# Kernel optimization log

Hardware: AMD Instinct MI355X
Metric: run time of the kernel (lower is better)

The kernel has to match this reference:

```python
import jax, jax.numpy as jnp
import numpy as np

N = 100000      # movie nodes
F_IN = 1024     # input feature dim
H, D = 8, 16    # heads, per-head dim (hidden = 128)
C = H * D       # hidden_channels = 128
E = 600000      # edges per metapath
P = 3           # number of metapath edge types
OUT = 3         # classes
NEG_SLOPE = 0.2


def setup_inputs() -> dict:
    key = jax.random.key(0)
    ks = jax.random.split(key, 10)
    return {
        "x_movie": jax.random.normal(ks[0], (N, F_IN), jnp.float32),
        "edge_index": jax.random.randint(ks[1], (P, 2, E), 0, N, jnp.int64),
        "W_proj": jax.random.normal(ks[2], (F_IN, C), jnp.float32) / np.sqrt(F_IN),
        "b_proj": jnp.zeros((C,), jnp.float32),
        "a_src": jax.random.normal(ks[3], (P, H, D), jnp.float32) / np.sqrt(D),
        "a_dst": jax.random.normal(ks[4], (P, H, D), jnp.float32) / np.sqrt(D),
        "k_W": jax.random.normal(ks[5], (C, C), jnp.float32) / np.sqrt(C),
        "k_b": jnp.zeros((C,), jnp.float32),
        "q": jax.random.normal(ks[6], (C,), jnp.float32) / np.sqrt(C),
        "lin_W": jax.random.normal(ks[7], (C, OUT), jnp.float32) / np.sqrt(C),
        "lin_b": jnp.zeros((OUT,), jnp.float32),
    }


def _metapath_attn(edge, asrc, adst, h):
    # edge: [2,E] int; asrc/adst: [H,D]; h: [N,H,D] projected node features
    n = h.shape[0]
    src, dst = edge[0], edge[1]
    al_s = (h * asrc).sum(-1)                 # [N,H]
    al_d = (h * adst).sum(-1)                 # [N,H]
    e = jax.nn.leaky_relu(al_s[src] + al_d[dst], NEG_SLOPE)  # [E,H]
    # per-destination softmax (numerically stable)
    m = jax.ops.segment_max(e, dst, num_segments=n)          # [N,H]
    p = jnp.exp(e - m[dst])
    denom = jax.ops.segment_sum(p, dst, num_segments=n)      # [N,H]
    alpha = p / (denom[dst] + 1e-16)                         # [E,H]
    msg = h[src] * alpha[..., None]                          # [E,H,D]
    out = jax.ops.segment_sum(msg, dst, num_segments=n)      # [N,H,D]
    return jax.nn.relu(out.reshape(n, H * D))                # [N,C]


def reference(x_movie, edge_index, W_proj, b_proj, a_src, a_dst, k_W, k_b, q, lin_W, lin_b):
    # shared node-type projection (dropout=0.6 omitted: eval mode)
    h = (x_movie @ W_proj + b_proj).reshape(N, H, D)         # [N,H,D]
    # per-metapath GAT attention, vmapped over the P metapath edge types
    outs = jax.vmap(_metapath_attn, in_axes=(0, 0, 0, None))(edge_index, a_src, a_dst, h)  # [P,N,C]
    # semantic attention fusion
    w = jnp.tanh(outs @ k_W + k_b).mean(axis=1)              # [P,C] mean over nodes
    score = (q * w).sum(-1)                                  # [P]
    beta = jax.nn.softmax(score)                             # [P]
    fused = (beta[:, None, None] * outs).sum(0)              # [N,C]
    return fused @ lin_W + lin_b                             # [N,OUT]
```

## Files before the change

### kernel.cpp

```cpp
#include <hip/hip_runtime.h>
#include <hip/hip_bf16.h>

#define NN 100000
#define FIN 1024
#define NH 8
#define ND 16
#define NC 128
#define NE 600000
#define NP 3
#define NOUT 3
#define NBLK 98

typedef __attribute__((ext_vector_type(8))) short bf16x8;
typedef __attribute__((ext_vector_type(4))) float f32x4;

__device__ __forceinline__ unsigned short f2bf(float f){
  union { __hip_bfloat16 b; unsigned short u; } cv;
  cv.b = __float2bfloat16(f);
  return cv.u;
}
__device__ __forceinline__ float bf2f(__hip_bfloat16 b){ return __bfloat162float(b); }
__device__ __forceinline__ float tanh_fast(float x){
  float e = __expf(2.0f*x);
  return 1.0f - 2.0f/(e + 1.0f);
}
__device__ __forceinline__ float lrelu(float x){ return x > 0.0f ? x : 0.2f*x; }

__global__ __launch_bounds__(256) void k_transpose_w(const float* __restrict__ W,
                                                     __hip_bfloat16* __restrict__ Wt){
  int t = blockIdx.x*256 + threadIdx.x;
  if (t >= FIN*NC) return;
  int k = t >> 7, c = t & 127;
  Wt[(size_t)c*FIN + k] = __float2bfloat16(W[t]);
}

__global__ __launch_bounds__(256) void k_proj(const float* __restrict__ x,
                                              const __hip_bfloat16* __restrict__ Wt,
                                              const float* __restrict__ bias,
                                              __hip_bfloat16* __restrict__ h){
  __shared__ __align__(16) __hip_bfloat16 As[64*40];
  __shared__ __align__(16) __hip_bfloat16 Bs[128*40];
  const int tid = threadIdx.x;
  const int wave = tid >> 6, lane = tid & 63;
  const int lr = lane & 15, lq = lane >> 4;
  const int m0 = blockIdx.x * 64;
  f32x4 acc[8] = {};
  for (int k0 = 0; k0 < FIN; k0 += 32){
#pragma unroll
    for (int i=0;i<2;i++){
      int idx = tid + 256*i;
      int row = idx >> 3, f4 = idx & 7;
      int gm = m0 + row; if (gm >= NN) gm = NN-1;
      const float4 v = *reinterpret_cast<const float4*>(x + (size_t)gm*FIN + k0 + f4*4);
      ushort4 pk; pk.x=f2bf(v.x); pk.y=f2bf(v.y); pk.z=f2bf(v.z); pk.w=f2bf(v.w);
      *reinterpret_cast<ushort4*>(&As[row*40 + f4*4]) = pk;
    }
#pragma unroll
    for (int i=0;i<2;i++){
      int idx = tid + 256*i;
      int c = idx >> 2, q = idx & 3;
      const uint4 v = *reinterpret_cast<const uint4*>(Wt + (size_t)c*FIN + k0 + q*8);
      *reinterpret_cast<uint4*>(&Bs[c*40 + q*8]) = v;
    }
    __syncthreads();
    bf16x8 afr = *reinterpret_cast<const bf16x8*>(&As[(wave*16 + lr)*40 + lq*8]);
#pragma unroll
    for (int t=0;t<8;t++){
      bf16x8 bfr = *reinterpret_cast<const bf16x8*>(&Bs[(t*16 + lr)*40 + lq*8]);
      acc[t] = __builtin_amdgcn_mfma_f32_16x16x32_bf16(afr, bfr, acc[t], 0, 0, 0);
    }
    __syncthreads();
  }
#pragma unroll
  for (int t=0;t<8;t++){
    int col = t*16 + lr;
    float bv = bias[col];
#pragma unroll
    for (int r=0;r<4;r++){
      int gm = m0 + wave*16 + lq*4 + r;
      if (gm < NN) h[(size_t)gm*NC + col] = __float2bfloat16(acc[t][r] + bv);
    }
  }
}

__global__ __launch_bounds__(256) void k_al(const __hip_bfloat16* __restrict__ h,
      const float* __restrict__ a_src, const float* __restrict__ a_dst,
      float* __restrict__ al_s, float* __restrict__ al_d){
  int t = blockIdx.x*256 + threadIdx.x;
  if (t >= NN*NH) return;
  int n = t >> 3, hh = t & 7;
  const __hip_bfloat16* hp = h + (size_t)n*NC + hh*ND;
  float hv[ND];
#pragma unroll
  for (int d=0; d<ND; d++) hv[d] = bf2f(hp[d]);
#pragma unroll
  for (int p=0;p<NP;p++){
    const float* as = a_src + (p*NH + hh)*ND;
    const float* ad = a_dst + (p*NH + hh)*ND;
    float ss=0.f, sd=0.f;
#pragma unroll
    for (int d=0;d<ND;d++){ ss += hv[d]*as[d]; sd += hv[d]*ad[d]; }
    al_s[((size_t)p*NN + n)*NH + hh] = ss;
    al_d[((size_t)p*NN + n)*NH + hh] = sd;
  }
}

__global__ __launch_bounds__(256) void k_deg(const int* __restrict__ edge,
                                             int* __restrict__ deg){
  int p = blockIdx.y;
  int e = blockIdx.x*256 + threadIdx.x;
  if (e >= NE) return;
  int dst = edge[(size_t)p*2*NE + NE + e];
  atomicAdd(&deg[p*NN + dst], 1);
}

__global__ __launch_bounds__(256) void k_scan_blk(const int* __restrict__ deg,
      int* __restrict__ row_start, int* __restrict__ blksum){
  __shared__ int sums[256];
  int p = blockIdx.y, blk = blockIdx.x, tid = threadIdx.x;
  int base = blk*1024 + tid*4;
  int v[4];
#pragma unroll
  for (int i=0;i<4;i++){
    int idx = base+i;
    v[i] = (idx < NN) ? deg[p*NN+idx] : 0;
  }
  int s = v[0]+v[1]+v[2]+v[3];
  sums[tid] = s;
  __syncthreads();
  for (int off=1; off<256; off<<=1){
    int t = (tid >= off) ? sums[tid-off] : 0;
    __syncthreads();
    sums[tid] += t;
    __syncthreads();
  }
  int run = sums[tid] - s;
  if (tid == 255) blksum[p*128 + blk] = sums[255];
  #pragma unroll
  for (int i=0;i<4;i++){
    int idx = base+i;
    if (idx < NN) row_start[p*(NN+1)+idx] = run;
    run += v[i];
  }
}

__global__ void k_scan_top(int* __restrict__ blksum){
  __shared__ int s[128];
  int p = blockIdx.x, tid = threadIdx.x;
  int v = (tid < NBLK) ? blksum[p*128+tid] : 0;
  s[tid] = v;
  __syncthreads();
  for (int off=1; off<128; off<<=1){
    int t = (tid>=off) ? s[tid-off] : 0;
    __syncthreads();
    s[tid] += t;
    __syncthreads();
  }
  blksum[p*128+tid] = s[tid] - v;
}

__global__ __launch_bounds__(256) void k_scan_add(int* __restrict__ row_start,
      const int* __restrict__ blksum, int* __restrict__ cursor){
  int p = blockIdx.y, blk = blockIdx.x, tid = threadIdx.x;
  int add = blksum[p*128+blk];
  int base = blk*1024 + tid*4;
#pragma unroll
  for (int i=0;i<4;i++){
    int idx = base+i;
    if (idx < NN){
      int vv = row_start[p*(NN+1)+idx] + add;
      row_start[p*(NN+1)+idx] = vv;
      cursor[p*NN+idx] = vv;
    }
  }
  if (blk==0 && tid==0) row_start[p*(NN+1)+NN] = NE;
}

__global__ __launch_bounds__(256) void k_fill(const int* __restrict__ edge,
      int* __restrict__ cursor, int* __restrict__ csr_src){
  int p = blockIdx.y;
  int e = blockIdx.x*256 + threadIdx.x;
  if (e >= NE) return;
  int src = edge[(size_t)p*2*NE + e];
  int dst = edge[(size_t)p*2*NE + NE + e];
  int pos = atomicAdd(&cursor[p*NN + dst], 1);
  csr_src[(size_t)p*NE + pos] = src;
}

__global__ __launch_bounds__(256) void k_gather(const int* __restrict__ row_start,
      const int* __restrict__ csr_src, const __hip_bfloat16* __restrict__ h,
      const float* __restrict__ al_s, const float* __restrict__ al_d,
      float* __restrict__ outs){
  int p = blockIdx.y;
  int dst = blockIdx.x*4 + (threadIdx.x >> 6);
  int lane = threadIdx.x & 63;
  if (dst >= NN) return;
  int hh = lane >> 3;
  int beg = row_start[p*(NN+1)+dst], end = row_start[p*(NN+1)+dst+1];
  float ald = al_d[((size_t)p*NN + dst)*NH + hh];
  const int*   cs  = csr_src + (size_t)p*NE;
  const float* als = al_s + (size_t)p*NN*NH;
  float denom = 0.f;
  for (int e=beg; e<end; e++){
    int src = cs[e];
    denom += __expf(lrelu(als[src*NH + hh] + ald));
  }
  float inv = 1.f/(denom + 1e-16f);
  float a0=0.f, a1=0.f;
  for (int e=beg; e<end; e++){
    int src = cs[e];
    float w = __expf(lrelu(als[src*NH + hh] + ald)) * inv;
    unsigned int hv = *reinterpret_cast<const unsigned int*>(h + (size_t)src*NC + lane*2);
    __hip_bfloat162 h2 = *reinterpret_cast<__hip_bfloat162*>(&hv);
    a0 += w * bf2f(h2.x);
    a1 += w * bf2f(h2.y);
  }
  float2 o; o.x = fmaxf(a0, 0.f); o.y = fmaxf(a1, 0.f);
  *reinterpret_cast<float2*>(outs + ((size_t)p*NN + dst)*NC + lane*2) = o;
}

__global__ __launch_bounds__(256) void k_semantic(const float* __restrict__ outs,
      const float* __restrict__ kW, const float* __restrict__ kb,
      float* __restrict__ wsum){
  __shared__ __align__(16) __hip_bfloat16 As[64*40];
  __shared__ __align__(16) __hip_bfloat16 Bs[128*136];
  __shared__ float wsum_s[NC];
  const int tid = threadIdx.x;
  const int wave = tid >> 6, lane = tid & 63;
  const int lr = lane & 15, lq = lane >> 4;
  const int p = blockIdx.y;
  const float* op = outs + (size_t)p*NN*NC;
  for (int i=tid; i<NC*NC; i+=256){
    int k = i >> 7, c = i & 127;
    Bs[c*136 + k] = __float2bfloat16(kW[i]);
  }
  if (tid < NC) wsum_s[tid] = 0.f;
  float kbv[8];
#pragma unroll
  for (int t=0;t<8;t++) kbv[t] = kb[t*16 + lr];
  float ps[8] = {};
  const int ntiles = (NN + 63)/64;
  for (int tile = blockIdx.x; tile < ntiles; tile += gridDim.x){
    const int m0 = tile*64;
    f32x4 acc[8] = {};
    for (int k0=0; k0<NC; k0+=32){
#pragma unroll
      for (int i=0;i<2;i++){
        int idx = tid + 256*i;
        int row = idx >> 3, f4 = idx & 7;
        int gm = m0 + row; if (gm >= NN) gm = NN-1;
        float4 v = *reinterpret_cast<const float4*>(op + (size_t)gm*NC + k0 + f4*4);
        ushort4 pk;
        pk.x=f2bf(v.x); pk.y=f2bf(v.y); pk.z=f2bf(v.z); pk.w=f2bf(v.w);
        *reinterpret_cast<ushort4*>(&As[row*40 + f4*4]) = pk;
      }
      __syncthreads();
      bf16x8 afr = *reinterpret_cast<const bf16x8*>(&As[(wave*16 + lr)*40 + lq*8]);
#pragma unroll
      for (int t=0;t<8;t++){
        bf16x8 bfr = *reinterpret_cast<const bf16x8*>(&Bs[(t*16 + lr)*136 + k0 + lq*8]);
        acc[t] = __builtin_amdgcn_mfma_f32_16x16x32_bf16(afr, bfr, acc[t], 0, 0, 0);
      }
      __syncthreads();
    }
#pragma unroll
    for (int t=0;t<8;t++){
#pragma unroll
      for (int r=0;r<4;r++){
        int gm = m0 + wave*16 + lq*4 + r;
        if (gm < NN) ps[t] += tanh_fast(acc[t][r] + kbv[t]);
      }
    }
  }
#pragma unroll
  for (int t=0;t<8;t++) atomicAdd(&wsum_s[t*16 + lr], ps[t]);
  __syncthreads();
  if (tid < NC) atomicAdd(&wsum[p*NC + tid], wsum_s[tid]);
}

__global__ void k_beta(const float* __restrict__ wsum, const float* __restrict__ qv,
                       float* __restrict__ beta){
  int lane = threadIdx.x;
  float s[NP];
#pragma unroll
  for (int p=0;p<NP;p++){
    float acc = wsum[p*NC + lane]*qv[lane] + wsum[p*NC + lane + 64]*qv[lane + 64];
#pragma unroll
    for (int off=32; off>0; off>>=1) acc += __shfl_down(acc, off);
    s[p] = acc;
  }
  if (lane == 0){
    float sc0 = s[0]/(float)NN, sc1 = s[1]/(float)NN, sc2 = s[2]/(float)NN;
    float mx = fmaxf(sc0, fmaxf(sc1, sc2));
    float e0 = __expf(sc0-mx), e1 = __expf(sc1-mx), e2 = __expf(sc2-mx);
    float inv = 1.0f/(e0+e1+e2);
    beta[0]=e0*inv; beta[1]=e1*inv; beta[2]=e2*inv;
  }
}

__global__ __launch_bounds__(256) void k_fuse(const float* __restrict__ outs,
      const float* __restrict__ beta, const float* __restrict__ linW,
      const float* __restrict__ linb, float* __restrict__ out){
  int node = blockIdx.x*4 + (threadIdx.x >> 6);
  int lane = threadIdx.x & 63;
  if (node >= NN) return;
  float b0 = beta[0], b1 = beta[1], b2 = beta[2];
  float a0=0.f, a1=0.f, a2=0.f;
#pragma unroll
  for (int i=0;i<2;i++){
    int c = lane + i*64;
    float f = b0*outs[((size_t)0*NN + node)*NC + c]
            + b1*outs[((size_t)1*NN + node)*NC + c]
            + b2*outs[((size_t)2*NN + node)*NC + c];
    a0 += f*linW[c*NOUT + 0];
    a1 += f*linW[c*NOUT + 1];
    a2 += f*linW[c*NOUT + 2];
  }
#pragma unroll
  for (int off=32; off>0; off>>=1){
    a0 += __shfl_down(a0, off);
    a1 += __shfl_down(a1, off);
    a2 += __shfl_down(a2, off);
  }
  if (lane == 0){
    out[(size_t)node*NOUT + 0] = a0 + linb[0];
    out[(size_t)node*NOUT + 1] = a1 + linb[1];
    out[(size_t)node*NOUT + 2] = a2 + linb[2];
  }
}

extern "C" void kernel_launch(void* const* d_in, const int* in_sizes, int n_in,
                              void* d_out, int out_size, void* d_ws, size_t ws_size,
                              hipStream_t stream){
  const float* x     = (const float*)d_in[0];
  const int*   edge  = (const int*)d_in[1];
  const float* Wp    = (const float*)d_in[2];
  const float* bp    = (const float*)d_in[3];
  const float* a_src = (const float*)d_in[4];
  const float* a_dst = (const float*)d_in[5];
  const float* kW    = (const float*)d_in[6];
  const float* kb    = (const float*)d_in[7];
  const float* qv    = (const float*)d_in[8];
  const float* linW  = (const float*)d_in[9];
  const float* linb  = (const float*)d_in[10];
  float* out = (float*)d_out;
  char* ws = (char*)d_ws;

  __hip_bfloat16* Wt  = (__hip_bfloat16*)(ws + 0);
  __hip_bfloat16* h   = (__hip_bfloat16*)(ws + 262144);
  float* al_s   = (float*)(ws + 25862144);
  float* al_d   = (float*)(ws + 35462144);
  int* deg      = (int*)(ws + 45062144);
  int* row_start= (int*)(ws + 46262144);
  int* blksum   = (int*)(ws + 47462160);
  int* csr_src  = (int*)(ws + 47463696);
  float* outs   = (float*)(ws + 54663696);
  float* wsum   = (float*)(ws + 208263696);
  float* beta   = (float*)(ws + 208265232);
  int* cursor   = deg;

  hipMemsetAsync(deg,  0, (size_t)NP*NN*4, stream);
  hipMemsetAsync(wsum, 0, NP*NC*4, stream);

  k_transpose_w<<<(FIN*NC + 255)/256, 256, 0, stream>>>(Wp, Wt);
  k_proj<<<(NN + 63)/64, 256, 0, stream>>>(x, Wt, bp, h);
  k_al<<<(NN*NH + 255)/256, 256, 0, stream>>>(h, a_src, a_dst, al_s, al_d);
  k_deg<<<dim3((NE + 255)/256, NP), 256, 0, stream>>>(edge, deg);
  k_scan_blk<<<dim3(NBLK, NP), 256, 0, stream>>>(deg, row_start, blksum);
  k_scan_top<<<NP, 128, 0, stream>>>(blksum);
  k_scan_add<<<dim3(NBLK, NP), 256, 0, stream>>>(row_start, blksum, cursor);
  k_fill<<<dim3((NE + 255)/256, NP), 256, 0, stream>>>(edge, cursor, csr_src);
  k_gather<<<dim3((NN + 3)/4, NP), 256, 0, stream>>>(row_start, csr_src, h, al_s, al_d, outs);
  k_semantic<<<dim3(256, NP), 256, 0, stream>>>(outs, kW, kb, wsum);
  k_beta<<<1, 64, 0, stream>>>(wsum, qv, beta);
  k_fuse<<<(NN + 3)/4, 256, 0, stream>>>(outs, beta, linW, linb, out);
}
```

Baseline: 1.291 ms.

## Store metapath outputs as bf16 and fuse gather softmax into single pass

The per-metapath attention outputs are now stored in bf16 instead of fp32, which halves the intermediate buffer traffic written by the gather kernel and read by the semantic and fuse kernels. The semantic kernel copies bf16 rows straight into shared memory without converting them. The gather kernel also merges its two edge loops into one unnormalized pass, dividing by the accumulated weight sum at the end and prefetching the next source index. This skips the max subtraction, which the code before also skipped, and adds bf16 rounding on the outputs.

```diff
diff --git a/kernel.cpp b/kernel.cpp
--- a/kernel.cpp
+++ b/kernel.cpp
@@ -190,7 +190,7 @@
 __global__ __launch_bounds__(256) void k_gather(const int* __restrict__ row_start,
       const int* __restrict__ csr_src, const __hip_bfloat16* __restrict__ h,
       const float* __restrict__ al_s, const float* __restrict__ al_d,
-      float* __restrict__ outs){
+      __hip_bfloat16* __restrict__ outs){
   int p = blockIdx.y;
   int dst = blockIdx.x*4 + (threadIdx.x >> 6);
   int lane = threadIdx.x & 63;
@@ -200,26 +200,26 @@
   float ald = al_d[((size_t)p*NN + dst)*NH + hh];
   const int*   cs  = csr_src + (size_t)p*NE;
   const float* als = al_s + (size_t)p*NN*NH;
-  float denom = 0.f;
+  float wsum = 0.f, a0 = 0.f, a1 = 0.f;
+  int src_next = (beg < end) ? cs[beg] : 0;
   for (int e=beg; e<end; e++){
-    int src = cs[e];
-    denom += __expf(lrelu(als[src*NH + hh] + ald));
-  }
-  float inv = 1.f/(denom + 1e-16f);
-  float a0=0.f, a1=0.f;
-  for (int e=beg; e<end; e++){
-    int src = cs[e];
-    float w = __expf(lrelu(als[src*NH + hh] + ald)) * inv;
+    int src = src_next;
+    if (e+1 < end) src_next = cs[e+1];
+    float w = __expf(lrelu(als[src*NH + hh] + ald));
     unsigned int hv = *reinterpret_cast<const unsigned int*>(h + (size_t)src*NC + lane*2);
     __hip_bfloat162 h2 = *reinterpret_cast<__hip_bfloat162*>(&hv);
+    wsum += w;
     a0 += w * bf2f(h2.x);
     a1 += w * bf2f(h2.y);
   }
-  float2 o; o.x = fmaxf(a0, 0.f); o.y = fmaxf(a1, 0.f);
-  *reinterpret_cast<float2*>(outs + ((size_t)p*NN + dst)*NC + lane*2) = o;
-}
-
-__global__ __launch_bounds__(256) void k_semantic(const float* __restrict__ outs,
+  float inv = 1.f/(wsum + 1e-16f);
+  unsigned short o0 = f2bf(fmaxf(a0*inv, 0.f));
+  unsigned short o1 = f2bf(fmaxf(a1*inv, 0.f));
+  unsigned int pk = (unsigned int)o0 | ((unsigned int)o1 << 16);
+  *reinterpret_cast<unsigned int*>(outs + ((size_t)p*NN + dst)*NC + lane*2) = pk;
+}
+
+__global__ __launch_bounds__(256) void k_semantic(const __hip_bfloat16* __restrict__ outs,
       const float* __restrict__ kW, const float* __restrict__ kb,
       float* __restrict__ wsum){
   __shared__ __align__(16) __hip_bfloat16 As[64*40];
@@ -229,7 +229,7 @@
   const int wave = tid >> 6, lane = tid & 63;
   const int lr = lane & 15, lq = lane >> 4;
   const int p = blockIdx.y;
-  const float* op = outs + (size_t)p*NN*NC;
+  const __hip_bfloat16* op = outs + (size_t)p*NN*NC;
   for (int i=tid; i<NC*NC; i+=256){
     int k = i >> 7, c = i & 127;
     Bs[c*136 + k] = __float2bfloat16(kW[i]);
@@ -244,15 +244,11 @@
     const int m0 = tile*64;
     f32x4 acc[8] = {};
     for (int k0=0; k0<NC; k0+=32){
-#pragma unroll
-      for (int i=0;i<2;i++){
-        int idx = tid + 256*i;
-        int row = idx >> 3, f4 = idx & 7;
+      {
+        int row = tid >> 2, q = tid & 3;
         int gm = m0 + row; if (gm >= NN) gm = NN-1;
-        float4 v = *reinterpret_cast<const float4*>(op + (size_t)gm*NC + k0 + f4*4);
-        ushort4 pk;
-        pk.x=f2bf(v.x); pk.y=f2bf(v.y); pk.z=f2bf(v.z); pk.w=f2bf(v.w);
-        *reinterpret_cast<ushort4*>(&As[row*40 + f4*4]) = pk;
+        const uint4 v = *reinterpret_cast<const uint4*>(op + (size_t)gm*NC + k0 + q*8);
+        *reinterpret_cast<uint4*>(&As[row*40 + q*8]) = v;
       }
       __syncthreads();
       bf16x8 afr = *reinterpret_cast<const bf16x8*>(&As[(wave*16 + lr)*40 + lq*8]);
@@ -298,24 +294,25 @@
   }
 }
 
-__global__ __launch_bounds__(256) void k_fuse(const float* __restrict__ outs,
+__global__ __launch_bounds__(256) void k_fuse(const __hip_bfloat16* __restrict__ outs,
       const float* __restrict__ beta, const float* __restrict__ linW,
       const float* __restrict__ linb, float* __restrict__ out){
   int node = blockIdx.x*4 + (threadIdx.x >> 6);
   int lane = threadIdx.x & 63;
   if (node >= NN) return;
   float b0 = beta[0], b1 = beta[1], b2 = beta[2];
-  float a0=0.f, a1=0.f, a2=0.f;
-#pragma unroll
-  for (int i=0;i<2;i++){
-    int c = lane + i*64;
-    float f = b0*outs[((size_t)0*NN + node)*NC + c]
-            + b1*outs[((size_t)1*NN + node)*NC + c]
-            + b2*outs[((size_t)2*NN + node)*NC + c];
-    a0 += f*linW[c*NOUT + 0];
-    a1 += f*linW[c*NOUT + 1];
-    a2 += f*linW[c*NOUT + 2];
-  }
+  unsigned int u0 = *reinterpret_cast<const unsigned int*>(outs + ((size_t)0*NN+node)*NC + lane*2);
+  unsigned int u1 = *reinterpret_cast<const unsigned int*>(outs + ((size_t)1*NN+node)*NC + lane*2);
+  unsigned int u2 = *reinterpret_cast<const unsigned int*>(outs + ((size_t)2*NN+node)*NC + lane*2);
+  __hip_bfloat162 v0 = *reinterpret_cast<__hip_bfloat162*>(&u0);
+  __hip_bfloat162 v1 = *reinterpret_cast<__hip_bfloat162*>(&u1);
+  __hip_bfloat162 v2 = *reinterpret_cast<__hip_bfloat162*>(&u2);
+  float f0 = b0*bf2f(v0.x) + b1*bf2f(v1.x) + b2*bf2f(v2.x);
+  float f1 = b0*bf2f(v0.y) + b1*bf2f(v1.y) + b2*bf2f(v2.y);
+  int c0 = lane*2, c1 = lane*2 + 1;
+  float a0 = f0*linW[c0*NOUT+0] + f1*linW[c1*NOUT+0];
+  float a1 = f0*linW[c0*NOUT+1] + f1*linW[c1*NOUT+1];
+  float a2 = f0*linW[c0*NOUT+2] + f1*linW[c1*NOUT+2];
 #pragma unroll
   for (int off=32; off>0; off>>=1){
     a0 += __shfl_down(a0, off);
@@ -354,9 +351,9 @@
   int* row_start= (int*)(ws + 46262144);
   int* blksum   = (int*)(ws + 47462160);
   int* csr_src  = (int*)(ws + 47463696);
-  float* outs   = (float*)(ws + 54663696);
-  float* wsum   = (float*)(ws + 208263696);
-  float* beta   = (float*)(ws + 208265232);
+  __hip_bfloat16* outs = (__hip_bfloat16*)(ws + 54663696);
+  float* wsum   = (float*)(ws + 131463696);
+  float* beta   = (float*)(ws + 131465232);
   int* cursor   = deg;
 
   hipMemsetAsync(deg,  0, (size_t)NP*NN*4, stream);
```

Result: faster. 1.081 ms (-16.3%).
